# Optimization experiments

Measured on AMD Instinct MI355X. Metric: run time of the kernel, lower is better.

Reference implementation:

```python
import jax, jax.numpy as jnp
import numpy as np

H = W = 224  # output confidence map size


def setup_inputs() -> dict:
    key = jax.random.key(0)
    k_x, k_w1, k_b1, k_w2, k_b2 = jax.random.split(key, 5)
    N = 500_000  # number of detections in the clip
    x = jax.random.uniform(k_x, (N, 7), dtype=jnp.float32)
    W1 = jax.random.normal(k_w1, (7, 64), dtype=jnp.float32) * (1.0 / np.sqrt(7.0))
    b1 = jax.random.normal(k_b1, (64,), dtype=jnp.float32) * 0.01
    W2 = jax.random.normal(k_w2, (64, H * W), dtype=jnp.float32) * (1.0 / 8.0)
    b2 = jax.random.normal(k_b2, (H * W,), dtype=jnp.float32) * 0.01
    return {"x": x, "W1": W1, "b1": b1, "W2": W2, "b2": b2}


def reference(x, W1, b1, W2, b2):
    # Encoder branch of Track_Block.forward:
    # silu -> Linear(7,64) -> silu -> mean over detections -> Linear(64,224*224)
    # -> silu -> reshape(224,224) -> clamp(0,1)
    h = jax.nn.silu(x)                       # [N, 7]
    h = jax.nn.silu(h @ W1 + b1)             # [N, 64]
    m = jnp.mean(h, axis=0)                  # [64] (mean over detection dim)
    e = jax.nn.silu(m @ W2 + b2)             # [50176]
    return jnp.clip(e.reshape(H, W), 0.0, 1.0)
```

## Files before the change

### kernel.cpp

```cpp
#include <hip/hip_runtime.h>

#define HWOUT 50176
#define NBLK1 512
#define CHUNK 1024
#define NWAVE 16
#define GRID2 196

typedef __attribute__((ext_vector_type(8))) short short8;
typedef __attribute__((ext_vector_type(4))) float f32x4;

__device__ __forceinline__ float fast_sigmoid(float x) {
    float t = __builtin_amdgcn_exp2f(-1.44269504088896340736f * x);
    return __builtin_amdgcn_rcpf(1.0f + t);
}
__device__ __forceinline__ float silu_f(float x) { return x * fast_sigmoid(x); }

__device__ __forceinline__ short to_bf16_bits(float f) {
    unsigned u = __builtin_bit_cast(unsigned, f);
    u += 0x7FFFu + ((u >> 16) & 1u);
    return (short)(u >> 16);
}

__global__ __launch_bounds__(1024) void k_stage1(const float* __restrict__ x,
                                                 const float* __restrict__ W1,
                                                 const float* __restrict__ b1,
                                                 float* __restrict__ partial,
                                                 int N) {
    __shared__ short xs[CHUNK * 8];
    __shared__ float red[NWAVE][64];
    const int t = threadIdx.x;
    const int lane = t & 63;
    const int wave = t >> 6;

    const int krow = (lane >> 4) * 8;
    const int c = lane & 15;
    short8 bf[4];
    f32x4 biasC[4];
#pragma unroll
    for (int g = 0; g < 4; ++g) {
#pragma unroll
        for (int j = 0; j < 8; ++j) {
            int k = krow + j;
            float v = (k < 7) ? W1[k * 64 + g * 16 + c] : 0.0f;
            bf[g][j] = to_bf16_bits(v);
        }
        float bb = b1[g * 16 + c];
        biasC[g] = (f32x4){bb, bb, bb, bb};
    }

    f32x4 accv[4];
#pragma unroll
    for (int g = 0; g < 4; ++g) accv[g] = (f32x4){0.0f, 0.0f, 0.0f, 0.0f};

    const int nchunk = (N + CHUNK - 1) / CHUNK;
    const short8 zero8 = {0, 0, 0, 0, 0, 0, 0, 0};
    const f32x4 onev = {1.0f, 1.0f, 1.0f, 1.0f};
    const f32x4 nlog2e = {-1.44269504088896f, -1.44269504088896f,
                          -1.44269504088896f, -1.44269504088896f};

    bool did_last = false;
    for (int ch = blockIdx.x; ch < nchunk; ch += NBLK1) {
        did_last |= (ch == nchunk - 1);
        const int row = ch * CHUNK + t;
        __syncthreads();
        {
            float v[7];
            if (row < N) {
#pragma unroll
                for (int k = 0; k < 7; ++k) v[k] = x[(size_t)row * 7 + k];
            } else {
#pragma unroll
                for (int k = 0; k < 7; ++k) v[k] = 0.0f;
            }
            short8 p;
#pragma unroll
            for (int k = 0; k < 7; ++k) p[k] = to_bf16_bits(silu_f(v[k]));
            p[7] = 0;
            *reinterpret_cast<short8*>(&xs[t * 8]) = p;
        }
        __syncthreads();

#pragma unroll
        for (int tt = 0; tt < 4; ++tt) {
            const int tile = wave * 4 + tt;
            short8 av = *reinterpret_cast<short8*>(&xs[(tile * 16 + c) * 8]);
            av = (lane < 16) ? av : zero8;
#pragma unroll
            for (int g = 0; g < 4; ++g) {
                f32x4 d = __builtin_amdgcn_mfma_f32_16x16x32_bf16(av, bf[g], biasC[g], 0, 0, 0);
                f32x4 targ = d * nlog2e;
                f32x4 ex;
                ex[0] = __builtin_amdgcn_exp2f(targ[0]);
                ex[1] = __builtin_amdgcn_exp2f(targ[1]);
                ex[2] = __builtin_amdgcn_exp2f(targ[2]);
                ex[3] = __builtin_amdgcn_exp2f(targ[3]);
                f32x4 den = ex + onev;
                f32x4 r;
                r[0] = __builtin_amdgcn_rcpf(den[0]);
                r[1] = __builtin_amdgcn_rcpf(den[1]);
                r[2] = __builtin_amdgcn_rcpf(den[2]);
                r[3] = __builtin_amdgcn_rcpf(den[3]);
                accv[g] = d * r + accv[g];
            }
        }
    }

    float accf[4];
#pragma unroll
    for (int g = 0; g < 4; ++g) {
        accf[g] = (accv[g][0] + accv[g][1]) + (accv[g][2] + accv[g][3]);
        accf[g] += __shfl_xor(accf[g], 16, 64);
        accf[g] += __shfl_xor(accf[g], 32, 64);
    }
    __syncthreads();
    if (lane < 16) {
#pragma unroll
        for (int g = 0; g < 4; ++g) red[wave][g * 16 + lane] = accf[g];
    }
    __syncthreads();
    if (t < 64) {
        float s = 0.0f;
#pragma unroll
        for (int wv = 0; wv < NWAVE; ++wv) s += red[wv][t];
        if (did_last) {
            const int phantom = nchunk * CHUNK - N;
            s -= (float)phantom * silu_f(b1[t]);
        }
        partial[blockIdx.x * 64 + t] = s;
    }
}

__global__ __launch_bounds__(1024) void k_out2(const float* __restrict__ partial,
                                               const float* __restrict__ W2,
                                               const float* __restrict__ b2,
                                               float* __restrict__ out,
                                               float invN) {
    __shared__ float4 red[1024];
    __shared__ float ml[64];
    __shared__ float osum[4][256];
    const int t = threadIdx.x;
    const int c4 = t & 15;
    const int grp = t >> 4;
    const float4* p4 = reinterpret_cast<const float4*>(partial);

    float4 s = {0.0f, 0.0f, 0.0f, 0.0f};
#pragma unroll
    for (int r = 0; r < NBLK1 / 64; ++r) {
        float4 v = p4[(grp + r * 64) * 16 + c4];
        s.x += v.x; s.y += v.y; s.z += v.z; s.w += v.w;
    }
    red[t] = s;
    __syncthreads();
    if (t < 256) {
        float4 a = red[t], b = red[t + 256], cc = red[t + 512], d = red[t + 768];
        a.x += b.x + cc.x + d.x;
        a.y += b.y + cc.y + d.y;
        a.z += b.z + cc.z + d.z;
        a.w += b.w + cc.w + d.w;
        red[t] = a;
    }
    __syncthreads();
    if (t < 16) {
        float4 a = {0.0f, 0.0f, 0.0f, 0.0f};
#pragma unroll
        for (int g = 0; g < 16; ++g) {
            float4 v = red[g * 16 + t];
            a.x += v.x; a.y += v.y; a.z += v.z; a.w += v.w;
        }
        ml[4 * t + 0] = a.x * invN;
        ml[4 * t + 1] = a.y * invN;
        ml[4 * t + 2] = a.z * invN;
        ml[4 * t + 3] = a.w * invN;
    }
    __syncthreads();

    const int s4 = t >> 8;
    const int i  = t & 255;
    const int j  = blockIdx.x * 256 + i;
    float a0 = 0.0f, a1 = 0.0f, a2 = 0.0f, a3 = 0.0f;
#pragma unroll
    for (int kk = 0; kk < 4; ++kk) {
        const int k = s4 * 16 + kk * 4;
        a0 = fmaf(ml[k + 0], W2[(size_t)(k + 0) * HWOUT + j], a0);
        a1 = fmaf(ml[k + 1], W2[(size_t)(k + 1) * HWOUT + j], a1);
        a2 = fmaf(ml[k + 2], W2[(size_t)(k + 2) * HWOUT + j], a2);
        a3 = fmaf(ml[k + 3], W2[(size_t)(k + 3) * HWOUT + j], a3);
    }
    osum[s4][i] = (a0 + a1) + (a2 + a3);
    __syncthreads();
    if (t < 256) {
        const int j2 = blockIdx.x * 256 + t;
        float e = osum[0][t] + osum[1][t] + osum[2][t] + osum[3][t] + b2[j2];
        e = silu_f(e);
        out[j2] = fminf(fmaxf(e, 0.0f), 1.0f);
    }
}

extern "C" void kernel_launch(void* const* d_in, const int* in_sizes, int n_in,
                              void* d_out, int out_size, void* d_ws, size_t ws_size,
                              hipStream_t stream) {
    const float* x  = (const float*)d_in[0];
    const float* W1 = (const float*)d_in[1];
    const float* b1 = (const float*)d_in[2];
    const float* W2 = (const float*)d_in[3];
    const float* b2 = (const float*)d_in[4];
    float* out = (float*)d_out;

    const int N = in_sizes[0] / 7;
    float* partial = (float*)d_ws;

    k_stage1<<<NBLK1, 1024, 0, stream>>>(x, W1, b1, partial, N);
    k_out2<<<GRID2, 1024, 0, stream>>>(partial, W2, b2, out, 1.0f / (float)N);
}
```

Before: 22.94 us.

## Fuse both stages into one cooperative kernel with a grid-wide sync

Merges the per-chunk MLP/mean stage and the output projection into one cooperative kernel launched with 256 blocks. A grid sync separates them, and each block then handles 196 output columns. This removes the second launch and the gap between kernels, at the cost of a grid-wide barrier and fewer blocks in stage one (256 instead of 512). Cooperative launch needs all 256 blocks of 1024 threads to be resident at once, and the larger shared-memory footprint could limit occupancy.

```diff
diff --git a/kernel.cpp b/kernel.cpp
--- a/kernel.cpp
+++ b/kernel.cpp
@@ -1,10 +1,13 @@
 #include <hip/hip_runtime.h>
+#include <hip/hip_cooperative_groups.h>
+
+namespace cg = cooperative_groups;
 
 #define HWOUT 50176
-#define NBLK1 512
+#define GRID  256
 #define CHUNK 1024
 #define NWAVE 16
-#define GRID2 196
+#define OUTPB 196
 
 typedef __attribute__((ext_vector_type(8))) short short8;
 typedef __attribute__((ext_vector_type(4))) float f32x4;
@@ -21,16 +24,21 @@
     return (short)(u >> 16);
 }
 
-__global__ __launch_bounds__(1024) void k_stage1(const float* __restrict__ x,
-                                                 const float* __restrict__ W1,
-                                                 const float* __restrict__ b1,
-                                                 float* __restrict__ partial,
-                                                 int N) {
+__global__ __launch_bounds__(1024) void k_fused(
+        const float* __restrict__ x,  const float* __restrict__ W1,
+        const float* __restrict__ b1, const float* __restrict__ W2,
+        const float* __restrict__ b2, float* __restrict__ out,
+        float* __restrict__ partial, int N, float invN) {
     __shared__ short xs[CHUNK * 8];
     __shared__ float red[NWAVE][64];
+    __shared__ float4 red4[1024];
+    __shared__ float ml[64];
+    __shared__ float osum[4][256];
+
     const int t = threadIdx.x;
     const int lane = t & 63;
     const int wave = t >> 6;
+    const int b = blockIdx.x;
 
     const int krow = (lane >> 4) * 8;
     const int c = lane & 15;
@@ -59,7 +67,7 @@
                           -1.44269504088896f, -1.44269504088896f};
 
     bool did_last = false;
-    for (int ch = blockIdx.x; ch < nchunk; ch += NBLK1) {
+    for (int ch = b; ch < nchunk; ch += GRID) {
         did_last |= (ch == nchunk - 1);
         const int row = ch * CHUNK + t;
         __syncthreads();
@@ -126,45 +134,38 @@
             const int phantom = nchunk * CHUNK - N;
             s -= (float)phantom * silu_f(b1[t]);
         }
-        partial[blockIdx.x * 64 + t] = s;
-    }
-}
-
-__global__ __launch_bounds__(1024) void k_out2(const float* __restrict__ partial,
-                                               const float* __restrict__ W2,
-                                               const float* __restrict__ b2,
-                                               float* __restrict__ out,
-                                               float invN) {
-    __shared__ float4 red[1024];
-    __shared__ float ml[64];
-    __shared__ float osum[4][256];
-    const int t = threadIdx.x;
-    const int c4 = t & 15;
-    const int grp = t >> 4;
-    const float4* p4 = reinterpret_cast<const float4*>(partial);
-
-    float4 s = {0.0f, 0.0f, 0.0f, 0.0f};
-#pragma unroll
-    for (int r = 0; r < NBLK1 / 64; ++r) {
-        float4 v = p4[(grp + r * 64) * 16 + c4];
-        s.x += v.x; s.y += v.y; s.z += v.z; s.w += v.w;
-    }
-    red[t] = s;
+        partial[b * 64 + t] = s;
+    }
+
+    cg::this_grid().sync();
+
+    {
+        const int c4 = t & 15;
+        const int grp = t >> 4;
+        const float4* p4 = reinterpret_cast<const float4*>(partial);
+        float4 s = {0.0f, 0.0f, 0.0f, 0.0f};
+#pragma unroll
+        for (int r = 0; r < GRID / 64; ++r) {
+            float4 v = p4[(grp + r * 64) * 16 + c4];
+            s.x += v.x; s.y += v.y; s.z += v.z; s.w += v.w;
+        }
+        red4[t] = s;
+    }
     __syncthreads();
     if (t < 256) {
-        float4 a = red[t], b = red[t + 256], cc = red[t + 512], d = red[t + 768];
-        a.x += b.x + cc.x + d.x;
-        a.y += b.y + cc.y + d.y;
-        a.z += b.z + cc.z + d.z;
-        a.w += b.w + cc.w + d.w;
-        red[t] = a;
+        float4 a = red4[t], bb = red4[t + 256], cc = red4[t + 512], d = red4[t + 768];
+        a.x += bb.x + cc.x + d.x;
+        a.y += bb.y + cc.y + d.y;
+        a.z += bb.z + cc.z + d.z;
+        a.w += bb.w + cc.w + d.w;
+        red4[t] = a;
     }
     __syncthreads();
     if (t < 16) {
         float4 a = {0.0f, 0.0f, 0.0f, 0.0f};
 #pragma unroll
         for (int g = 0; g < 16; ++g) {
-            float4 v = red[g * 16 + t];
+            float4 v = red4[g * 16 + t];
             a.x += v.x; a.y += v.y; a.z += v.z; a.w += v.w;
         }
         ml[4 * t + 0] = a.x * invN;
@@ -174,25 +175,29 @@
     }
     __syncthreads();
 
-    const int s4 = t >> 8;
-    const int i  = t & 255;
-    const int j  = blockIdx.x * 256 + i;
-    float a0 = 0.0f, a1 = 0.0f, a2 = 0.0f, a3 = 0.0f;
-#pragma unroll
-    for (int kk = 0; kk < 4; ++kk) {
-        const int k = s4 * 16 + kk * 4;
-        a0 = fmaf(ml[k + 0], W2[(size_t)(k + 0) * HWOUT + j], a0);
-        a1 = fmaf(ml[k + 1], W2[(size_t)(k + 1) * HWOUT + j], a1);
-        a2 = fmaf(ml[k + 2], W2[(size_t)(k + 2) * HWOUT + j], a2);
-        a3 = fmaf(ml[k + 3], W2[(size_t)(k + 3) * HWOUT + j], a3);
-    }
-    osum[s4][i] = (a0 + a1) + (a2 + a3);
-    __syncthreads();
-    if (t < 256) {
-        const int j2 = blockIdx.x * 256 + t;
-        float e = osum[0][t] + osum[1][t] + osum[2][t] + osum[3][t] + b2[j2];
+    {
+        const int s4 = t >> 8;
+        const int i = t & 255;
+        float a0 = 0.0f, a1 = 0.0f, a2 = 0.0f, a3 = 0.0f;
+        if (i < OUTPB) {
+            const int j = b * OUTPB + i;
+#pragma unroll
+            for (int kk = 0; kk < 4; ++kk) {
+                const int k = s4 * 16 + kk * 4;
+                a0 = fmaf(ml[k + 0], W2[(size_t)(k + 0) * HWOUT + j], a0);
+                a1 = fmaf(ml[k + 1], W2[(size_t)(k + 1) * HWOUT + j], a1);
+                a2 = fmaf(ml[k + 2], W2[(size_t)(k + 2) * HWOUT + j], a2);
+                a3 = fmaf(ml[k + 3], W2[(size_t)(k + 3) * HWOUT + j], a3);
+            }
+        }
+        osum[s4][i] = (a0 + a1) + (a2 + a3);
+    }
+    __syncthreads();
+    if (t < OUTPB) {
+        const int j = b * OUTPB + t;
+        float e = osum[0][t] + osum[1][t] + osum[2][t] + osum[3][t] + b2[j];
         e = silu_f(e);
-        out[j2] = fminf(fmaxf(e, 0.0f), 1.0f);
+        out[j] = fminf(fmaxf(e, 0.0f), 1.0f);
     }
 }
 
@@ -206,9 +211,12 @@
     const float* b2 = (const float*)d_in[4];
     float* out = (float*)d_out;
 
-    const int N = in_sizes[0] / 7;
+    int N = in_sizes[0] / 7;
+    float invN = 1.0f / (float)N;
     float* partial = (float*)d_ws;
 
-    k_stage1<<<NBLK1, 1024, 0, stream>>>(x, W1, b1, partial, N);
-    k_out2<<<GRID2, 1024, 0, stream>>>(partial, W2, b2, out, 1.0f / (float)N);
-}
+    void* args[] = {(void*)&x, (void*)&W1, (void*)&b1, (void*)&W2, (void*)&b2,
+                    (void*)&out, (void*)&partial, (void*)&N, (void*)&invN};
+    hipLaunchCooperativeKernel((const void*)k_fused, dim3(GRID), dim3(1024),
+                               args, 0, stream);
+}
```

Result: slower. 53.89 us (+134.9%).
